# Optimization experiments

Hardware: AMD Instinct MI355X
Metric: run time of the kernel (lower is better)

Reference implementation:

```python
import jax, jax.numpy as jnp
import numpy as np

B, T, C, K, TNEI = 16, 1024, 1024, 8, 2
H = int(C * 1.5)  # FeedForward hidden = int(1.5*in_dim)
EPS = 1e-5


def setup_inputs() -> dict:
    key = jax.random.key(0)
    ks = jax.random.split(key, 16)
    ws = C ** -0.5  # fan-in style init scale for projections
    return {
        "x": jax.random.normal(ks[0], (B, T, C), jnp.float32),
        "radj": jax.random.uniform(ks[1], (B, T, K), jnp.float32),
        "inxs": jax.random.randint(ks[2], (B, T, K), 0, T),
        "Wq": jax.random.normal(ks[3], (C, C), jnp.float32) * ws,
        "Wk": jax.random.normal(ks[4], (C, C), jnp.float32) * ws,
        "Wv": jax.random.normal(ks[5], (C, C), jnp.float32) * ws,
        "Wo": jax.random.normal(ks[6], (C, C), jnp.float32) * ws,
        "ln1_g": jnp.ones((C,), jnp.float32),
        "ln1_b": jnp.zeros((C,), jnp.float32),
        "W1": jax.random.normal(ks[7], (C, H), jnp.float32) * ws,
        "b1": jnp.zeros((H,), jnp.float32),
        "W2": jax.random.normal(ks[8], (H, C), jnp.float32) * (H ** -0.5),
        "b2": jnp.zeros((C,), jnp.float32),
        "ln2_g": jnp.ones((C,), jnp.float32),
        "ln2_b": jnp.zeros((C,), jnp.float32),
    }


def _layernorm(x, g, b):
    mu = jnp.mean(x, axis=-1, keepdims=True)
    var = jnp.mean(jnp.square(x - mu), axis=-1, keepdims=True)
    return (x - mu) * jax.lax.rsqrt(var + EPS) * g + b


def reference(x, radj, inxs, Wq, Wk, Wv, Wo, ln1_g, ln1_b, W1, b1, W2, b2, ln2_g, ln2_b):
    scale = 1.0 / jnp.sqrt(jnp.asarray(C, x.dtype))
    gather = jax.vmap(lambda a, i: a[i])  # (T,C),(T,K) -> (T,K,C), vmapped over B

    # MBasicReason: tnei hops of top-k neighbor attention (adjacency-biased)
    h = x
    for _ in range(TNEI):
        q = h @ Wq                                  # (B,T,C)
        kn = gather(h @ Wk, inxs)                   # (B,T,K,C)
        vn = gather(h @ Wv, inxs)                   # (B,T,K,C)
        scores = jnp.einsum('btc,btkc->btk', q, kn) * scale + radj
        attn = jax.nn.softmax(scores, axis=-1)      # (B,T,K); dropout off (eval)
        h = jnp.einsum('btk,btkc->btc', attn, vn) @ Wo

    # residual + LN, FFN, residual + LN
    y = _layernorm(x + jax.nn.relu(h), ln1_g, ln1_b)
    f = jax.nn.relu(y @ W1 + b1) @ W2 + b2
    return _layernorm(y + f, ln2_g, ln2_b)
```

## Files before the change

### kernel.cpp

```cpp
#include <hip/hip_runtime.h>
#include <hip/hip_bf16.h>
#include <cstddef>
#include <cstdint>

#define B_    16
#define T_    1024
#define C_    1024
#define K_    8
#define H_    1536
#define TNEI_ 2
static constexpr float EPS_ = 1e-5f;

typedef __attribute__((ext_vector_type(8))) short bf16x8;
typedef __attribute__((ext_vector_type(4))) float f32x4;

__device__ __forceinline__ float bf2f(unsigned short u) {
    return __uint_as_float(((unsigned)u) << 16);
}
__device__ __forceinline__ unsigned short f2bf(float f) {
    __hip_bfloat16 h = __float2bfloat16(f);
    union { __hip_bfloat16 h; unsigned short u; } cvt;
    cvt.h = h;
    return cvt.u;
}

__device__ __forceinline__ void gload_lds16(const void* g, void* l) {
    __builtin_amdgcn_global_load_lds(
        (const __attribute__((address_space(1))) void*)g,
        (__attribute__((address_space(3))) void*)l,
        16, 0, 0);
}

#define VMCNT0 asm volatile("s_waitcnt vmcnt(0)" ::: "memory")
#define VMCNT4 asm volatile("s_waitcnt vmcnt(4)" ::: "memory")
#define BARRIER do {                                   \
    __builtin_amdgcn_sched_barrier(0);                 \
    __builtin_amdgcn_s_barrier();                      \
    asm volatile("" ::: "memory");                     \
    __builtin_amdgcn_sched_barrier(0);                 \
} while (0)

__global__ __launch_bounds__(256) void f2bf_kernel(
    const float* __restrict__ in, unsigned short* __restrict__ out)
{
    const size_t i = (size_t)blockIdx.x * 256 + threadIdx.x;
    const float4 v = *reinterpret_cast<const float4*>(&in[i * 4]);
    ushort4 o;
    o.x = f2bf(v.x); o.y = f2bf(v.y); o.z = f2bf(v.z); o.w = f2bf(v.w);
    *reinterpret_cast<ushort4*>(&out[i * 4]) = o;
}

__global__ __launch_bounds__(256) void wtrans_kernel(
    const float* __restrict__ W, unsigned short* __restrict__ WT, int R, int Cc)
{
    __shared__ float t[32][33];
    const int c0 = blockIdx.x * 32, r0 = blockIdx.y * 32;
    const int tx = threadIdx.x & 31, ty = threadIdx.x >> 5;
    #pragma unroll
    for (int i = 0; i < 4; ++i)
        t[ty + 8 * i][tx] = W[(size_t)(r0 + ty + 8 * i) * Cc + c0 + tx];
    __syncthreads();
    #pragma unroll
    for (int i = 0; i < 4; ++i)
        WT[(size_t)(c0 + ty + 8 * i) * R + r0 + tx] = f2bf(t[tx][ty + 8 * i]);
}

template <int OUT_BF16, int BIAS, int RELU>
__global__ __launch_bounds__(512, 2) void gemm_bt_kernel(
    const unsigned short* __restrict__ A, const unsigned short* __restrict__ Bt,
    const float* __restrict__ bias, void* __restrict__ Cout,
    int M, int N, int K)
{
    constexpr int BK = 32;
    __shared__ unsigned short smem[3 * 16384];

    const int tid  = threadIdx.x;
    const int lane = tid & 63;
    const int wid  = tid >> 6;
    const int wm   = wid >> 2, wn = wid & 3;

    const int nwg  = gridDim.x * gridDim.y;
    int bidl = blockIdx.y * gridDim.x + blockIdx.x;
    bidl = (bidl & 7) * (nwg >> 3) + (bidl >> 3);
    const int bx = bidl % gridDim.x;
    const int by = bidl / gridDim.x;
    const int row0 = by * 256;
    const int col0 = bx * 256;

    const int NT = K >> 5;

    const int sub = lane >> 2;
    const int kk  = (((lane & 3) ^ ((lane >> 3) & 3))) * 8;

    f32x4 acc[8][4] = {};

    auto stage = [&](int kt, int bufi) {
        unsigned short* As = smem + bufi * 16384;
        unsigned short* Bs = As + 8192;
        #pragma unroll
        for (int i = 0; i < 2; ++i) {
            const int cg = i * 8 + wid;
            const int r = cg * 16 + sub;
            gload_lds16(&A[(size_t)(row0 + r) * K + kt + kk], &As[cg * 512]);
        }
        #pragma unroll
        for (int i = 0; i < 2; ++i) {
            const int cg = i * 8 + wid;
            const int r = cg * 16 + sub;
            gload_lds16(&Bt[(size_t)(col0 + r) * K + kt + kk], &Bs[cg * 512]);
        }
    };

    const int slot = ((lane >> 4) ^ ((lane >> 1) & 3)) * 8;
    auto loadfrag = [&](int bufi, bf16x8* a, bf16x8* b) {
        const unsigned short* As = smem + bufi * 16384;
        const unsigned short* Bs = As + 8192;
        #pragma unroll
        for (int m = 0; m < 8; ++m) {
            const int r = wm * 128 + m * 16 + (lane & 15);
            a[m] = *reinterpret_cast<const bf16x8*>(&As[r * 32 + slot]);
        }
        #pragma unroll
        for (int n = 0; n < 4; ++n) {
            const int c = wn * 64 + n * 16 + (lane & 15);
            b[n] = *reinterpret_cast<const bf16x8*>(&Bs[c * 32 + slot]);
        }
    };

    auto mfma32 = [&](const bf16x8* a, const bf16x8* b) {
        __builtin_amdgcn_s_setprio(1);
        #pragma unroll
        for (int m = 0; m < 8; ++m)
            #pragma unroll
            for (int n = 0; n < 4; ++n)
                acc[m][n] = __builtin_amdgcn_mfma_f32_16x16x32_bf16(
                    a[m], b[n], acc[m][n], 0, 0, 0);
        __builtin_amdgcn_s_setprio(0);
    };

    bf16x8 fa[8], fb[4];

    stage(0, 0);
    stage(BK, 1);
    VMCNT4;
    BARRIER;
    loadfrag(0, fa, fb);

    int bs = 2, br = 1;
    for (int t = 0; t < NT; ++t) {
        if (t + 2 < NT) stage((t + 2) * BK, bs);
        if (++bs == 3) bs = 0;
        mfma32(fa, fb);
        if (t + 1 < NT) {
            if (t + 2 < NT) { VMCNT4; } else { VMCNT0; }
            BARRIER;
            loadfrag(br, fa, fb);
        }
        if (++br == 3) br = 0;
    }

    if (OUT_BF16) {
        char* tile = (char*)smem;
        #pragma unroll
        for (int p = 0; p < 2; ++p) {
            __syncthreads();
            #pragma unroll
            for (int m4 = 0; m4 < 4; ++m4) {
                const int m = p * 4 + m4;
                #pragma unroll
                for (int n = 0; n < 4; ++n) {
                    const int cc = wn * 64 + n * 16 + (lane & 15);
                    const float bv = BIAS ? bias[col0 + cc] : 0.0f;
                    #pragma unroll
                    for (int r = 0; r < 4; ++r) {
                        const int lrow = wm * 64 + m4 * 16 + (lane >> 4) * 4 + r;
                        float v = acc[m][n][r] + bv;
                        if (RELU) v = fmaxf(v, 0.0f);
                        const int byte = (lrow * 512 + cc * 2) ^ (((lrow >> 2) & 3) << 5);
                        *reinterpret_cast<unsigned short*>(tile + byte) = f2bf(v);
                    }
                }
            }
            __syncthreads();
            const int cchunk = tid & 31;
            const int rbase  = tid >> 5;
            #pragma unroll
            for (int it = 0; it < 8; ++it) {
                const int lr = it * 16 + rbase;
                const int byte = (lr * 512 + cchunk * 16) ^ (((lr >> 2) & 3) << 5);
                const uint4 v = *reinterpret_cast<const uint4*>(tile + byte);
                const int grow = row0 + (lr >> 6) * 128 + p * 64 + (lr & 63);
                *reinterpret_cast<uint4*>(
                    &((unsigned short*)Cout)[(size_t)grow * N + col0 + cchunk * 8]) = v;
            }
        }
    } else {
        #pragma unroll
        for (int m = 0; m < 8; ++m) {
            #pragma unroll
            for (int n = 0; n < 4; ++n) {
                const int cg = col0 + wn * 64 + n * 16 + (lane & 15);
                const float bv = BIAS ? bias[cg] : 0.0f;
                #pragma unroll
                for (int r = 0; r < 4; ++r) {
                    const int rg = row0 + wm * 128 + m * 16 + (lane >> 4) * 4 + r;
                    float v = acc[m][n][r] + bv;
                    if (RELU) v = fmaxf(v, 0.0f);
                    ((float*)Cout)[(size_t)rg * N + cg] = v;
                }
            }
        }
    }
}

__global__ __launch_bounds__(256) void attn_kernel(
    const unsigned short* __restrict__ qkv, const int* __restrict__ inxs,
    const float* __restrict__ radj, unsigned short* __restrict__ out)
{
    const int bt  = blockIdx.x;
    const int b   = bt >> 10;
    const int tid = threadIdx.x;
    const float scale = 0.03125f;

    __shared__ int   s_idx[K_];
    __shared__ float s_sc[K_];
    __shared__ float red[K_][4];

    if (tid < K_) s_idx[tid] = inxs[bt * K_ + tid];
    __syncthreads();

    const ushort4 qv = *reinterpret_cast<const ushort4*>(
        &qkv[(size_t)bt * 3072 + tid * 4]);
    const float qf[4] = { bf2f(qv.x), bf2f(qv.y), bf2f(qv.z), bf2f(qv.w) };

    float part[K_];
    #pragma unroll
    for (int k = 0; k < K_; ++k) {
        const size_t nb = (size_t)b * T_ + s_idx[k];
        const ushort4 kv = *reinterpret_cast<const ushort4*>(
            &qkv[nb * 3072 + 1024 + tid * 4]);
        part[k] = qf[0] * bf2f(kv.x) + qf[1] * bf2f(kv.y)
                + qf[2] * bf2f(kv.z) + qf[3] * bf2f(kv.w);
    }

    const int lane = tid & 63, wid = tid >> 6;
    #pragma unroll
    for (int k = 0; k < K_; ++k) {
        float v = part[k];
        #pragma unroll
        for (int off = 32; off; off >>= 1) v += __shfl_xor(v, off);
        if (lane == 0) red[k][wid] = v;
    }
    __syncthreads();
    if (tid < K_) {
        s_sc[tid] = (red[tid][0] + red[tid][1] + red[tid][2] + red[tid][3]) * scale
                    + radj[bt * K_ + tid];
    }
    __syncthreads();

    float m = s_sc[0];
    #pragma unroll
    for (int k = 1; k < K_; ++k) m = fmaxf(m, s_sc[k]);
    float w[K_], wsum = 0.f;
    #pragma unroll
    for (int k = 0; k < K_; ++k) { w[k] = expf(s_sc[k] - m); wsum += w[k]; }
    const float inv = 1.0f / wsum;

    float o[4] = {0.f, 0.f, 0.f, 0.f};
    #pragma unroll
    for (int k = 0; k < K_; ++k) {
        const size_t nb = (size_t)b * T_ + s_idx[k];
        const ushort4 vv = *reinterpret_cast<const ushort4*>(
            &qkv[nb * 3072 + 2048 + tid * 4]);
        const float wk = w[k] * inv;
        o[0] = fmaf(wk, bf2f(vv.x), o[0]);
        o[1] = fmaf(wk, bf2f(vv.y), o[1]);
        o[2] = fmaf(wk, bf2f(vv.z), o[2]);
        o[3] = fmaf(wk, bf2f(vv.w), o[3]);
    }
    ushort4 ov;
    ov.x = f2bf(o[0]); ov.y = f2bf(o[1]); ov.z = f2bf(o[2]); ov.w = f2bf(o[3]);
    *reinterpret_cast<ushort4*>(&out[(size_t)bt * C_ + tid * 4]) = ov;
}

template <int RELU, int WB>
__global__ __launch_bounds__(256) void ln_residual_kernel(
    const float* __restrict__ a, const float* __restrict__ bb,
    const float* __restrict__ g, const float* __restrict__ beta,
    float* __restrict__ out, unsigned short* __restrict__ outb)
{
    const int bt  = blockIdx.x;
    const int tid = threadIdx.x;

    const float4 av = *reinterpret_cast<const float4*>(&a[(size_t)bt * C_ + tid * 4]);
    const float4 bv = *reinterpret_cast<const float4*>(&bb[(size_t)bt * C_ + tid * 4]);
    float4 s;
    s.x = av.x + (RELU ? fmaxf(bv.x, 0.f) : bv.x);
    s.y = av.y + (RELU ? fmaxf(bv.y, 0.f) : bv.y);
    s.z = av.z + (RELU ? fmaxf(bv.z, 0.f) : bv.z);
    s.w = av.w + (RELU ? fmaxf(bv.w, 0.f) : bv.w);

    float sum = s.x + s.y + s.z + s.w;
    float sq  = s.x * s.x + s.y * s.y + s.z * s.z + s.w * s.w;

    const int lane = tid & 63, wid = tid >> 6;
    __shared__ float rs[4], rq[4];
    #pragma unroll
    for (int off = 32; off; off >>= 1) {
        sum += __shfl_xor(sum, off);
        sq  += __shfl_xor(sq,  off);
    }
    if (lane == 0) { rs[wid] = sum; rq[wid] = sq; }
    __syncthreads();
    sum = rs[0] + rs[1] + rs[2] + rs[3];
    sq  = rq[0] + rq[1] + rq[2] + rq[3];

    const float mu  = sum * (1.0f / C_);
    const float var = sq * (1.0f / C_) - mu * mu;
    const float r   = rsqrtf(var + EPS_);

    const float4 gv = *reinterpret_cast<const float4*>(&g[tid * 4]);
    const float4 be = *reinterpret_cast<const float4*>(&beta[tid * 4]);
    float4 o;
    o.x = (s.x - mu) * r * gv.x + be.x;
    o.y = (s.y - mu) * r * gv.y + be.y;
    o.z = (s.z - mu) * r * gv.z + be.z;
    o.w = (s.w - mu) * r * gv.w + be.w;
    *reinterpret_cast<float4*>(&out[(size_t)bt * C_ + tid * 4]) = o;
    if (WB) {
        ushort4 ob;
        ob.x = f2bf(o.x); ob.y = f2bf(o.y); ob.z = f2bf(o.z); ob.w = f2bf(o.w);
        *reinterpret_cast<ushort4*>(&outb[(size_t)bt * C_ + tid * 4]) = ob;
    }
}

extern "C" void kernel_launch(void* const* d_in, const int* in_sizes, int n_in,
                              void* d_out, int out_size, void* d_ws, size_t ws_size,
                              hipStream_t stream)
{
    const float* x     = (const float*)d_in[0];
    const float* radj  = (const float*)d_in[1];
    const int*   inxs  = (const int*)  d_in[2];
    const float* Wq    = (const float*)d_in[3];
    const float* Wk    = (const float*)d_in[4];
    const float* Wv    = (const float*)d_in[5];
    const float* Wo    = (const float*)d_in[6];
    const float* ln1_g = (const float*)d_in[7];
    const float* ln1_b = (const float*)d_in[8];
    const float* W1    = (const float*)d_in[9];
    const float* b1    = (const float*)d_in[10];
    const float* W2    = (const float*)d_in[11];
    const float* b2    = (const float*)d_in[12];
    const float* ln2_g = (const float*)d_in[13];
    const float* ln2_b = (const float*)d_in[14];
    float* out = (float*)d_out;

    char* wsb = (char*)d_ws;
    const size_t MB = 1 << 20;
    unsigned short* WqkvT = (unsigned short*)(wsb + 0 * MB);
    unsigned short* WoT   = (unsigned short*)(wsb + 6 * MB);
    unsigned short* W1T   = (unsigned short*)(wsb + 8 * MB);
    unsigned short* W2T   = (unsigned short*)(wsb + 11 * MB);
    unsigned short* xb  = (unsigned short*)(wsb + 16 * MB);
    unsigned short* hb  = xb;
    unsigned short* qkv = (unsigned short*)(wsb + 48 * MB);
    unsigned short* ab  = (unsigned short*)(wsb + 144 * MB);
    float*          h2  = (float*)(wsb + 48 * MB);
    float*          y   = (float*)(wsb + 112 * MB);
    unsigned short* yb  = (unsigned short*)(wsb + 176 * MB);
    unsigned short* hid = (unsigned short*)(wsb + 208 * MB);
    float*          f   = (float*)(wsb + 48 * MB);

    const int M = B_ * T_;
    const dim3 blk(256);
    const dim3 blkG(512);
    const dim3 gQKV(3 * C_ / 256, M / 256);
    const dim3 gC(C_ / 256, M / 256);
    const dim3 gH(H_ / 256, M / 256);

    wtrans_kernel<<<dim3(32, 32), blk, 0, stream>>>(Wq, WqkvT,                C_, C_);
    wtrans_kernel<<<dim3(32, 32), blk, 0, stream>>>(Wk, WqkvT + 1024 * 1024,  C_, C_);
    wtrans_kernel<<<dim3(32, 32), blk, 0, stream>>>(Wv, WqkvT + 2048 * 1024,  C_, C_);
    wtrans_kernel<<<dim3(32, 32), blk, 0, stream>>>(Wo, WoT, C_, C_);
    wtrans_kernel<<<dim3(48, 32), blk, 0, stream>>>(W1, W1T, C_, H_);
    wtrans_kernel<<<dim3(32, 48), blk, 0, stream>>>(W2, W2T, H_, C_);
    f2bf_kernel<<<dim3((size_t)M * C_ / 1024), blk, 0, stream>>>(x, xb);

    for (int hop = 0; hop < TNEI_; ++hop) {
        const unsigned short* hin = (hop == 0) ? xb : hb;
        gemm_bt_kernel<1, 0, 0><<<gQKV, blkG, 0, stream>>>(hin, WqkvT, nullptr, qkv,
                                                           M, 3 * C_, C_);
        attn_kernel<<<dim3(M), blk, 0, stream>>>(qkv, inxs, radj, ab);
        if (hop == 0)
            gemm_bt_kernel<1, 0, 0><<<gC, blkG, 0, stream>>>(ab, WoT, nullptr, hb,
                                                             M, C_, C_);
        else
            gemm_bt_kernel<0, 0, 0><<<gC, blkG, 0, stream>>>(ab, WoT, nullptr, h2,
                                                             M, C_, C_);
    }

    ln_residual_kernel<1, 1><<<dim3(M), blk, 0, stream>>>(x, h2, ln1_g, ln1_b, y, yb);
    gemm_bt_kernel<1, 1, 1><<<gH, blkG, 0, stream>>>(yb,  W1T, b1, hid, M, H_, C_);
    gemm_bt_kernel<0, 1, 0><<<gC, blkG, 0, stream>>>(hid, W2T, b2, f,   M, C_, H_);
    ln_residual_kernel<0, 0><<<dim3(M), blk, 0, stream>>>(y, f, ln2_g, ln2_b, out, nullptr);
}
```

Baseline: 789.6 us.

## Use one wavefront per token in attention and emit bf16 GEMM outputs

The attention kernel now assigns one 64-lane wavefront per token, four tokens per block. Each lane handles 16 channels with 16-byte loads, the reductions use only wave shuffles, and the shared-memory barriers are gone. The final Wo GEMM and the W2 GEMM now write bf16 instead of fp32, and the layernorm kernels read that bf16. This halves those intermediate writes and reads, at the cost of bf16 rounding on the residual inputs before layernorm.

```diff
diff --git a/kernel.cpp b/kernel.cpp
--- a/kernel.cpp
+++ b/kernel.cpp
@@ -217,75 +217,100 @@
     const unsigned short* __restrict__ qkv, const int* __restrict__ inxs,
     const float* __restrict__ radj, unsigned short* __restrict__ out)
 {
-    const int bt  = blockIdx.x;
-    const int b   = bt >> 10;
-    const int tid = threadIdx.x;
+    const int wv   = threadIdx.x >> 6;
+    const int lane = threadIdx.x & 63;
+    const int bt   = blockIdx.x * 4 + wv;
+    const int b    = bt >> 10;
     const float scale = 0.03125f;
 
-    __shared__ int   s_idx[K_];
-    __shared__ float s_sc[K_];
-    __shared__ float red[K_][4];
-
-    if (tid < K_) s_idx[tid] = inxs[bt * K_ + tid];
-    __syncthreads();
-
-    const ushort4 qv = *reinterpret_cast<const ushort4*>(
-        &qkv[(size_t)bt * 3072 + tid * 4]);
-    const float qf[4] = { bf2f(qv.x), bf2f(qv.y), bf2f(qv.z), bf2f(qv.w) };
-
-    float part[K_];
+    const unsigned short* qr = &qkv[(size_t)bt * 3072 + lane * 16];
+    const bf16x8 q0 = *reinterpret_cast<const bf16x8*>(qr);
+    const bf16x8 q1 = *reinterpret_cast<const bf16x8*>(qr + 8);
+    float qf[16];
+    #pragma unroll
+    for (int j = 0; j < 8; ++j) {
+        qf[j]     = bf2f((unsigned short)q0[j]);
+        qf[j + 8] = bf2f((unsigned short)q1[j]);
+    }
+
+    int   iv = 0;
+    float rv = 0.f;
+    if (lane < K_) {
+        iv = inxs[bt * K_ + lane];
+        rv = radj[bt * K_ + lane];
+    }
+
+    float s[K_];
     #pragma unroll
     for (int k = 0; k < K_; ++k) {
-        const size_t nb = (size_t)b * T_ + s_idx[k];
-        const ushort4 kv = *reinterpret_cast<const ushort4*>(
-            &qkv[nb * 3072 + 1024 + tid * 4]);
-        part[k] = qf[0] * bf2f(kv.x) + qf[1] * bf2f(kv.y)
-                + qf[2] * bf2f(kv.z) + qf[3] * bf2f(kv.w);
-    }
-
-    const int lane = tid & 63, wid = tid >> 6;
+        const int idx = __shfl(iv, k);
+        const unsigned short* kr =
+            &qkv[((size_t)b * T_ + idx) * 3072 + 1024 + lane * 16];
+        const bf16x8 k0 = *reinterpret_cast<const bf16x8*>(kr);
+        const bf16x8 k1 = *reinterpret_cast<const bf16x8*>(kr + 8);
+        float d = 0.f;
+        #pragma unroll
+        for (int j = 0; j < 8; ++j) {
+            d = fmaf(qf[j],     bf2f((unsigned short)k0[j]), d);
+            d = fmaf(qf[j + 8], bf2f((unsigned short)k1[j]), d);
+        }
+        s[k] = d;
+    }
+    #pragma unroll
+    for (int off = 1; off < 64; off <<= 1) {
+        #pragma unroll
+        for (int k = 0; k < K_; ++k) s[k] += __shfl_xor(s[k], off);
+    }
+
+    float sc[K_];
+    #pragma unroll
+    for (int k = 0; k < K_; ++k) sc[k] = s[k] * scale + __shfl(rv, k);
+
+    float m = sc[0];
+    #pragma unroll
+    for (int k = 1; k < K_; ++k) m = fmaxf(m, sc[k]);
+    float w[K_], wsum = 0.f;
+    #pragma unroll
+    for (int k = 0; k < K_; ++k) { w[k] = __expf(sc[k] - m); wsum += w[k]; }
+    const float inv = 1.0f / wsum;
+
+    float o[16] = {};
     #pragma unroll
     for (int k = 0; k < K_; ++k) {
-        float v = part[k];
-        #pragma unroll
-        for (int off = 32; off; off >>= 1) v += __shfl_xor(v, off);
-        if (lane == 0) red[k][wid] = v;
-    }
-    __syncthreads();
-    if (tid < K_) {
-        s_sc[tid] = (red[tid][0] + red[tid][1] + red[tid][2] + red[tid][3]) * scale
-                    + radj[bt * K_ + tid];
-    }
-    __syncthreads();
-
-    float m = s_sc[0];
-    #pragma unroll
-    for (int k = 1; k < K_; ++k) m = fmaxf(m, s_sc[k]);
-    float w[K_], wsum = 0.f;
-    #pragma unroll
-    for (int k = 0; k < K_; ++k) { w[k] = expf(s_sc[k] - m); wsum += w[k]; }
-    const float inv = 1.0f / wsum;
-
-    float o[4] = {0.f, 0.f, 0.f, 0.f};
-    #pragma unroll
-    for (int k = 0; k < K_; ++k) {
-        const size_t nb = (size_t)b * T_ + s_idx[k];
-        const ushort4 vv = *reinterpret_cast<const ushort4*>(
-            &qkv[nb * 3072 + 2048 + tid * 4]);
+        const int idx = __shfl(iv, k);
+        const unsigned short* vr =
+            &qkv[((size_t)b * T_ + idx) * 3072 + 2048 + lane * 16];
+        const bf16x8 v0 = *reinterpret_cast<const bf16x8*>(vr);
+        const bf16x8 v1 = *reinterpret_cast<const bf16x8*>(vr + 8);
         const float wk = w[k] * inv;
-        o[0] = fmaf(wk, bf2f(vv.x), o[0]);
-        o[1] = fmaf(wk, bf2f(vv.y), o[1]);
-        o[2] = fmaf(wk, bf2f(vv.z), o[2]);
-        o[3] = fmaf(wk, bf2f(vv.w), o[3]);
-    }
-    ushort4 ov;
-    ov.x = f2bf(o[0]); ov.y = f2bf(o[1]); ov.z = f2bf(o[2]); ov.w = f2bf(o[3]);
-    *reinterpret_cast<ushort4*>(&out[(size_t)bt * C_ + tid * 4]) = ov;
+        #pragma unroll
+        for (int j = 0; j < 8; ++j) {
+            o[j]     = fmaf(wk, bf2f((unsigned short)v0[j]), o[j]);
+            o[j + 8] = fmaf(wk, bf2f((unsigned short)v1[j]), o[j + 8]);
+        }
+    }
+    ushort4 pk[2];
+    #pragma unroll
+    for (int h = 0; h < 2; ++h) {
+        pk[h].x = f2bf(o[h * 8 + 0]); pk[h].y = f2bf(o[h * 8 + 1]);
+        pk[h].z = f2bf(o[h * 8 + 2]); pk[h].w = f2bf(o[h * 8 + 3]);
+    }
+    ushort4 pk2[2];
+    #pragma unroll
+    for (int h = 0; h < 2; ++h) {
+        pk2[h].x = f2bf(o[h * 8 + 4]); pk2[h].y = f2bf(o[h * 8 + 5]);
+        pk2[h].z = f2bf(o[h * 8 + 6]); pk2[h].w = f2bf(o[h * 8 + 7]);
+    }
+    unsigned short* op = &out[(size_t)bt * C_ + lane * 16];
+    *reinterpret_cast<ushort4*>(op + 0)  = pk[0];
+    *reinterpret_cast<ushort4*>(op + 4)  = pk2[0];
+    *reinterpret_cast<ushort4*>(op + 8)  = pk[1];
+    *reinterpret_cast<ushort4*>(op + 12) = pk2[1];
 }
 
 template <int RELU, int WB>
 __global__ __launch_bounds__(256) void ln_residual_kernel(
-    const float* __restrict__ a, const float* __restrict__ bb,
+    const float* __restrict__ a, const unsigned short* __restrict__ bb,
     const float* __restrict__ g, const float* __restrict__ beta,
     float* __restrict__ out, unsigned short* __restrict__ outb)
 {
@@ -293,7 +318,8 @@
     const int tid = threadIdx.x;
 
     const float4 av = *reinterpret_cast<const float4*>(&a[(size_t)bt * C_ + tid * 4]);
-    const float4 bv = *reinterpret_cast<const float4*>(&bb[(size_t)bt * C_ + tid * 4]);
+    const ushort4 bu = *reinterpret_cast<const ushort4*>(&bb[(size_t)bt * C_ + tid * 4]);
+    float4 bv = make_float4(bf2f(bu.x), bf2f(bu.y), bf2f(bu.z), bf2f(bu.w));
     float4 s;
     s.x = av.x + (RELU ? fmaxf(bv.x, 0.f) : bv.x);
     s.y = av.y + (RELU ? fmaxf(bv.y, 0.f) : bv.y);
@@ -365,11 +391,11 @@
     unsigned short* hb  = xb;
     unsigned short* qkv = (unsigned short*)(wsb + 48 * MB);
     unsigned short* ab  = (unsigned short*)(wsb + 144 * MB);
-    float*          h2  = (float*)(wsb + 48 * MB);
+    unsigned short* h2b = (unsigned short*)(wsb + 48 * MB);
+    unsigned short* fb  = (unsigned short*)(wsb + 80 * MB);
     float*          y   = (float*)(wsb + 112 * MB);
     unsigned short* yb  = (unsigned short*)(wsb + 176 * MB);
     unsigned short* hid = (unsigned short*)(wsb + 208 * MB);
-    float*          f   = (float*)(wsb + 48 * MB);
 
     const int M = B_ * T_;
     const dim3 blk(256);
@@ -390,17 +416,17 @@
         const unsigned short* hin = (hop == 0) ? xb : hb;
         gemm_bt_kernel<1, 0, 0><<<gQKV, blkG, 0, stream>>>(hin, WqkvT, nullptr, qkv,
                                                            M, 3 * C_, C_);
-        attn_kernel<<<dim3(M), blk, 0, stream>>>(qkv, inxs, radj, ab);
+        attn_kernel<<<dim3(M / 4), blk, 0, stream>>>(qkv, inxs, radj, ab);
         if (hop == 0)
             gemm_bt_kernel<1, 0, 0><<<gC, blkG, 0, stream>>>(ab, WoT, nullptr, hb,
                                                              M, C_, C_);
         else
-            gemm_bt_kernel<0, 0, 0><<<gC, blkG, 0, stream>>>(ab, WoT, nullptr, h2,
+            gemm_bt_kernel<1, 0, 0><<<gC, blkG, 0, stream>>>(ab, WoT, nullptr, h2b,
                                                              M, C_, C_);
     }
 
-    ln_residual_kernel<1, 1><<<dim3(M), blk, 0, stream>>>(x, h2, ln1_g, ln1_b, y, yb);
+    ln_residual_kernel<1, 1><<<dim3(M), blk, 0, stream>>>(x, h2b, ln1_g, ln1_b, y, yb);
     gemm_bt_kernel<1, 1, 1><<<gH, blkG, 0, stream>>>(yb,  W1T, b1, hid, M, H_, C_);
-    gemm_bt_kernel<0, 1, 0><<<gC, blkG, 0, stream>>>(hid, W2T, b2, f,   M, C_, H_);
-    ln_residual_kernel<0, 0><<<dim3(M), blk, 0, stream>>>(y, f, ln2_g, ln2_b, out, nullptr);
-}
+    gemm_bt_kernel<1, 1, 0><<<gC, blkG, 0, stream>>>(hid, W2T, b2, fb,  M, C_, H_);
+    ln_residual_kernel<0, 0><<<dim3(M), blk, 0, stream>>>(y, fb, ln2_g, ln2_b, out, nullptr);
+}
```

Measured after the change: 764.8 us. 3.2% less time.
